# Kernel tuning notes

Hardware: AMD Instinct MI355X
Metric: run time of the kernel (lower is better)

Reference implementation:

```python
import jax, jax.numpy as jnp
import numpy as np


def setup_inputs() -> dict:
    key = jax.random.key(0)
    ks = jax.random.split(key, 8)
    B, C, H, W = 8, 256, 64, 64
    s = 1.0 / np.sqrt(C)
    return {
        "x": jax.random.normal(ks[0], (B, C, H, W), dtype=jnp.float32),
        "wq": jax.random.normal(ks[1], (C, C), dtype=jnp.float32) * s,
        "bq": jax.random.normal(ks[2], (C,), dtype=jnp.float32) * 0.01,
        "wk": jax.random.normal(ks[3], (C, C), dtype=jnp.float32) * s,
        "bk": jax.random.normal(ks[4], (C,), dtype=jnp.float32) * 0.01,
        "wv": jax.random.normal(ks[5], (C, C), dtype=jnp.float32) * s,
        "bv": jax.random.normal(ks[6], (C,), dtype=jnp.float32) * 0.01,
        "gamma": jax.random.normal(ks[7], (1,), dtype=jnp.float32) * 0.1,
    }


def reference(x, wq, bq, wk, bk, wv, bv, gamma):
    B, C, H, W = x.shape
    N = H * W
    xf = x.reshape(B, C, N)  # flatten spatial -> tokens
    # 1x1 convs == per-pixel linear maps over channels
    q = jnp.einsum('oc,bcn->bon', wq, xf) + bq[None, :, None]  # [B,C,N]
    k = jnp.einsum('oc,bcn->bon', wk, xf) + bk[None, :, None]  # [B,C,N]
    v = jnp.einsum('oc,bcn->bon', wv, xf) + bv[None, :, None]  # [B,C,N]
    # energy[b,n,m] = <q[:, n], k[:, m]>  (query tokens x key tokens)
    energy = jnp.einsum('bcn,bcm->bnm', q, k)  # [B,N,N]
    attention = jax.nn.softmax(energy, axis=-1)
    # out = V @ attention^T : out[b,c,n] = sum_m v[b,c,m] * attention[b,n,m]
    out = jnp.einsum('bcm,bnm->bcn', v, attention).reshape(B, C, H, W)
    return gamma[0] * out + x
```

## Files before the change

kernel.cpp:

```cpp
#include <hip/hip_runtime.h>
#include <hip/hip_bf16.h>
#include <cstdint>


typedef short short8 __attribute__((ext_vector_type(8)));
typedef short short4v __attribute__((ext_vector_type(4)));
typedef float f32x4 __attribute__((ext_vector_type(4)));

#define MFMA16(a, b, c) __builtin_amdgcn_mfma_f32_16x16x32_bf16((a), (b), (c), 0, 0, 0)
#define LOG2E 1.4426950408889634f

__device__ __forceinline__ unsigned short f2bf(float f) {
    union { float f; unsigned int u; } v;
    v.f = f;
    unsigned int u = v.u;
    return (unsigned short)((u + 0x7fffu + ((u >> 16) & 1u)) >> 16);
}

__device__ __forceinline__ void load_lds16(const unsigned short* g, unsigned short* l) {
    __builtin_amdgcn_global_load_lds(
        (const __attribute__((address_space(1))) unsigned int*)g,
        (__attribute__((address_space(3))) unsigned int*)l, 16, 0, 0);
}

__device__ __forceinline__ float rowmax16_dpp(float x) {
    int v;
    v = __builtin_amdgcn_update_dpp(0, __float_as_int(x), 0x121, 0xf, 0xf, false);
    x = fmaxf(x, __int_as_float(v));
    v = __builtin_amdgcn_update_dpp(0, __float_as_int(x), 0x122, 0xf, 0xf, false);
    x = fmaxf(x, __int_as_float(v));
    v = __builtin_amdgcn_update_dpp(0, __float_as_int(x), 0x124, 0xf, 0xf, false);
    x = fmaxf(x, __int_as_float(v));
    v = __builtin_amdgcn_update_dpp(0, __float_as_int(x), 0x128, 0xf, 0xf, false);
    x = fmaxf(x, __int_as_float(v));
    return x;
}

__global__ __launch_bounds__(256) void wcvt_kernel(
    const float* __restrict__ wq, const float* __restrict__ wk,
    const float* __restrict__ wv, unsigned short* __restrict__ Wb)
{
    int idx = (blockIdx.x * 256 + threadIdx.x) * 4;
    const float* src = (idx < 65536) ? wq : ((idx < 131072) ? wk : wv);
    float4 f = *(const float4*)(src + (idx & 65535));
    short4v s = { (short)f2bf(f.x), (short)f2bf(f.y), (short)f2bf(f.z), (short)f2bf(f.w) };
    *(short4v*)(Wb + idx) = s;
}

__global__ __launch_bounds__(256, 2) void qkv_kernel(
    const float* __restrict__ x, const unsigned short* __restrict__ Wb,
    const float* __restrict__ bq, const float* __restrict__ bk,
    const float* __restrict__ bv,
    unsigned short* __restrict__ Qc, unsigned short* __restrict__ Kr,
    unsigned short* __restrict__ Vc)
{
    const int C = 256, N = 4096;
    __shared__ __align__(16) unsigned short Xt[32][264];

    const int tid  = threadIdx.x;
    const int bid  = blockIdx.x;
    const int b    = bid >> 7;
    const int n0   = (bid & 127) * 32;
    const int wave = tid >> 6;
    const int lane = tid & 63;
    const int quad = lane >> 4;
    const int l16  = lane & 15;
    const int ch0  = wave * 64;

    {
        const int token = tid & 31;
        const int cg    = tid >> 5;
        const float* xb = x + ((size_t)b * C) * N + n0 + token;
#pragma unroll
        for (int p = 0; p < 8; p++) {
            int c0 = p * 32 + cg * 4;
            float f0 = xb[(size_t)(c0 + 0) * N];
            float f1 = xb[(size_t)(c0 + 1) * N];
            float f2 = xb[(size_t)(c0 + 2) * N];
            float f3 = xb[(size_t)(c0 + 3) * N];
            short4v s = { (short)f2bf(f0), (short)f2bf(f1), (short)f2bf(f2), (short)f2bf(f3) };
            *(short4v*)(&Xt[token][c0]) = s;
        }
    }
    __syncthreads();

    f32x4 acc[3][4][2];
#pragma unroll
    for (int m = 0; m < 3; m++)
#pragma unroll
        for (int ct = 0; ct < 4; ct++)
#pragma unroll
            for (int tt = 0; tt < 2; tt++) acc[m][ct][tt] = (f32x4){0.f, 0.f, 0.f, 0.f};

#pragma unroll
    for (int kc = 0; kc < 8; kc++) {
        const int ko = kc * 32 + quad * 8;
        short8 ax0 = *(const short8*)(&Xt[l16][ko]);
        short8 ax1 = *(const short8*)(&Xt[16 + l16][ko]);
#pragma unroll
        for (int m = 0; m < 3; m++) {
#pragma unroll
            for (int ct = 0; ct < 4; ct++) {
                short8 wf = *(const short8*)(Wb + ((size_t)m << 16) +
                                             (ch0 + ct * 16 + l16) * 256 + ko);
                acc[m][ct][0] = MFMA16(ax0, wf, acc[m][ct][0]);
                acc[m][ct][1] = MFMA16(ax1, wf, acc[m][ct][1]);
            }
        }
    }

#pragma unroll
    for (int ct = 0; ct < 4; ct++) {
        const int ch = ch0 + ct * 16 + l16;
        const float biq = bq[ch], biv = bv[ch];
#pragma unroll
        for (int tt = 0; tt < 2; tt++) {
            const int tok0 = n0 + tt * 16 + quad * 4;
            short4v qs = { (short)f2bf((acc[0][ct][tt][0] + biq) * LOG2E),
                           (short)f2bf((acc[0][ct][tt][1] + biq) * LOG2E),
                           (short)f2bf((acc[0][ct][tt][2] + biq) * LOG2E),
                           (short)f2bf((acc[0][ct][tt][3] + biq) * LOG2E) };
            *(short4v*)(Qc + ((size_t)b * C + ch) * N + tok0) = qs;
            short4v vs = { (short)f2bf(acc[2][ct][tt][0] + biv),
                           (short)f2bf(acc[2][ct][tt][1] + biv),
                           (short)f2bf(acc[2][ct][tt][2] + biv),
                           (short)f2bf(acc[2][ct][tt][3] + biv) };
            *(short4v*)(Vc + ((size_t)b * C + ch) * N + tok0) = vs;
        }
    }

    __syncthreads();
#pragma unroll
    for (int ct = 0; ct < 4; ct++) {
        const int ch = ch0 + ct * 16 + l16;
        const float bik = bk[ch];
#pragma unroll
        for (int tt = 0; tt < 2; tt++) {
#pragma unroll
            for (int r = 0; r < 4; r++)
                Xt[tt * 16 + quad * 4 + r][ch] = f2bf(acc[1][ct][tt][r] + bik);
        }
    }
    __syncthreads();
#pragma unroll
    for (int p = 0; p < 2; p++) {
        int chunk = p * 256 + tid;
        int tok = chunk >> 4;
        int cc  = (chunk & 15) * 16;
        *(short8*)(Kr + ((size_t)b * N + n0 + tok) * C + cc) = *(const short8*)(&Xt[tok][cc]);
    }
}

__global__ __launch_bounds__(512, 2) void attn_kernel(
    const unsigned short* __restrict__ Qc,
    const unsigned short* __restrict__ Kr,
    const unsigned short* __restrict__ Vc,
    const float* __restrict__ x,
    const float* __restrict__ gamma,
    float* __restrict__ out)
{
    const int C = 256, N = 4096;
    __shared__ __align__(16) unsigned short KV[2][32768];
    __shared__ __align__(16) unsigned short Pt[8][1280];
    __shared__ float MlL[4][32];
    __shared__ float MwL[4];

    const int tid  = threadIdx.x;
    const int wave = tid >> 6;
    const int ks   = wave >> 2;
    const int w4   = wave & 3;
    const int lane = tid & 63;
    const int quad = lane >> 4;
    const int l16  = lane & 15;
    const int bid  = blockIdx.x;
    const int b    = bid & 7;
    const int q0   = (bid >> 3) * 128 + w4 * 32;

    const unsigned short* kb  = Kr + (size_t)b * N * C;
    const unsigned short* vcb = Vc + (size_t)b * C * N;

    short8 aqL[8], aqH[8];
    {
        const unsigned short* qb = Qc + (size_t)b * C * N + q0 + l16;
#pragma unroll
        for (int f = 0; f < 8; f++) {
#pragma unroll
            for (int j = 0; j < 8; j++) {
                size_t co = (size_t)(f * 32 + quad * 8 + j) * N;
                aqL[f][j] = (short)qb[co];
                aqH[f][j] = (short)qb[co + 16];
            }
        }
    }

    f32x4 oL[16], oH[16];
#pragma unroll
    for (int t = 0; t < 16; t++) {
        oL[t] = (f32x4){0.f, 0.f, 0.f, 0.f};
        oH[t] = (f32x4){0.f, 0.f, 0.f, 0.f};
    }
    float m_w = -__builtin_inff();
    float l_p[2][4];
#pragma unroll
    for (int h = 0; h < 2; h++)
#pragma unroll
        for (int r = 0; r < 4; r++) l_p[h][r] = 0.f;

    auto stage = [&](int buf, int m0) {
        unsigned short* dst = &KV[buf][0];
#pragma unroll
        for (int p = 0; p < 4; p++) {
            int chunk = p * 512 + tid;
            int half = chunk >> 10;
            int idx  = chunk & 1023;
            int key = idx >> 5;
            int j = (idx & 31) ^ (key & 31);
            load_lds16(kb + (size_t)(half * 2048 + m0 + key) * C + j * 8,
                       dst + half * 16384 + idx * 8);
        }
#pragma unroll
        for (int p = 0; p < 4; p++) {
            int chunk = p * 512 + tid;
            int half = chunk >> 10;
            int idx  = chunk & 1023;
            int c = idx >> 2;
            int j = (idx & 3) ^ (c & 3);
            load_lds16(vcb + (size_t)c * N + half * 2048 + m0 + j * 8,
                       dst + half * 16384 + 8192 + idx * 8);
        }
    };

    stage(0, 0);
    __syncthreads();

    unsigned short* PtW = &Pt[wave][0];

    for (int it = 0; it < 64; ++it) {
        const int cur = it & 1;
        if (it < 63) stage(cur ^ 1, (it + 1) * 32);

        const unsigned short* Kb = &KV[cur][ks * 16384];
        const unsigned short* Vb = Kb + 8192;

        f32x4 sL0 = {0.f,0.f,0.f,0.f}, sL1 = {0.f,0.f,0.f,0.f};
        f32x4 sH0 = {0.f,0.f,0.f,0.f}, sH1 = {0.f,0.f,0.f,0.f};
#pragma unroll
        for (int f = 0; f < 8; f++) {
            const int j = f * 4 + quad;
            int k0 = l16, k1 = 16 + l16;
            short8 kf0 = *(const short8*)(Kb + (k0 * 32 + (j ^ (k0 & 31))) * 8);
            short8 kf1 = *(const short8*)(Kb + (k1 * 32 + (j ^ (k1 & 31))) * 8);
            sL0 = MFMA16(aqL[f], kf0, sL0);
            sL1 = MFMA16(aqL[f], kf1, sL1);
            sH0 = MFMA16(aqH[f], kf0, sH0);
            sH1 = MFMA16(aqH[f], kf1, sH1);
        }

        float mx = fmaxf(fmaxf(fmaxf(sL0[0], sL0[1]), fmaxf(sL0[2], sL0[3])),
                         fmaxf(fmaxf(sL1[0], sL1[1]), fmaxf(sL1[2], sL1[3])));
        mx = fmaxf(mx, fmaxf(fmaxf(fmaxf(sH0[0], sH0[1]), fmaxf(sH0[2], sH0[3])),
                             fmaxf(fmaxf(sH1[0], sH1[1]), fmaxf(sH1[2], sH1[3]))));
        mx = rowmax16_dpp(mx);
        mx = fmaxf(mx, __shfl_xor(mx, 16));
        mx = fmaxf(mx, __shfl_xor(mx, 32));
        const float mn = fmaxf(m_w, mx);
        const float al = exp2f(m_w - mn);
        const bool up = mn > m_w;
        m_w = mn;

#pragma unroll
        for (int r = 0; r < 4; r++) {
            {
                float e0 = exp2f(sL0[r] - mn);
                float e1 = exp2f(sL1[r] - mn);
                l_p[0][r] = l_p[0][r] * al + (e0 + e1);
                union { __hip_bfloat162 v; unsigned int u; } cv;
                cv.v = __float22bfloat162_rn(float2{e0, e1});
                unsigned short* pr = PtW + (quad * 4 + r) * 40 + l16;
                pr[0]  = (unsigned short)(cv.u & 0xffff);
                pr[16] = (unsigned short)(cv.u >> 16);
            }
            {
                float e0 = exp2f(sH0[r] - mn);
                float e1 = exp2f(sH1[r] - mn);
                l_p[1][r] = l_p[1][r] * al + (e0 + e1);
                union { __hip_bfloat162 v; unsigned int u; } cv;
                cv.v = __float22bfloat162_rn(float2{e0, e1});
                unsigned short* pr = PtW + (16 + quad * 4 + r) * 40 + l16;
                pr[0]  = (unsigned short)(cv.u & 0xffff);
                pr[16] = (unsigned short)(cv.u >> 16);
            }
        }
        if (up) {
#pragma unroll
            for (int t = 0; t < 16; t++) { oL[t] *= al; oH[t] *= al; }
        }

        short8 apL = *(const short8*)(PtW + l16 * 40 + quad * 8);
        short8 apH = *(const short8*)(PtW + (16 + l16) * 40 + quad * 8);

#pragma unroll
        for (int t = 0; t < 16; t++) {
            int c = t * 16 + l16;
            short8 vf = *(const short8*)(Vb + (c * 4 + (quad ^ (c & 3))) * 8);
            oL[t] = MFMA16(apL, vf, oL[t]);
            oH[t] = MFMA16(apH, vf, oH[t]);
        }
        __syncthreads();
    }

#pragma unroll
    for (int h = 0; h < 2; h++)
#pragma unroll
        for (int r = 0; r < 4; r++) {
            float rs = l_p[h][r];
            rs += __shfl_xor(rs, 1);
            rs += __shfl_xor(rs, 2);
            rs += __shfl_xor(rs, 4);
            rs += __shfl_xor(rs, 8);
            l_p[h][r] = rs;
        }

    float* CombF = (float*)(&KV[0][0]);
    __syncthreads();
    if (ks == 1) {
#pragma unroll
        for (int t = 0; t < 16; t++) {
#pragma unroll
            for (int r = 0; r < 4; r++) {
                CombF[(size_t)(w4 * 32 + quad * 4 + r) * 256 + t * 16 + l16] = oL[t][r];
                CombF[(size_t)(w4 * 32 + 16 + quad * 4 + r) * 256 + t * 16 + l16] = oH[t][r];
            }
        }
        if (l16 == 0) {
#pragma unroll
            for (int h = 0; h < 2; h++)
#pragma unroll
                for (int r = 0; r < 4; r++)
                    MlL[w4][h * 16 + quad * 4 + r] = l_p[h][r];
            if (lane == 0) MwL[w4] = m_w;
        }
    }
    __syncthreads();
    if (ks == 0) {
        const float g = gamma[0];
        const float m2w = MwL[w4];
        const float mt = fmaxf(m_w, m2w);
        const float f1 = exp2f(m_w - mt);
        const float f2 = exp2f(m2w - mt);
        float linv[2][4];
#pragma unroll
        for (int h = 0; h < 2; h++)
#pragma unroll
            for (int r = 0; r < 4; r++) {
                float l2 = MlL[w4][h * 16 + quad * 4 + r];
                linv[h][r] = g / (l_p[h][r] * f1 + l2 * f2);
            }
#pragma unroll
        for (int t = 0; t < 16; t++) {
            const int c = t * 16 + l16;
#pragma unroll
            for (int h = 0; h < 2; h++) {
                const int nb = q0 + h * 16 + quad * 4;
                f32x4 o1 = h ? oH[t] : oL[t];
                f32x4 ov;
#pragma unroll
                for (int r = 0; r < 4; r++) {
                    float o2 = CombF[(size_t)(w4 * 32 + h * 16 + quad * 4 + r) * 256 + c];
                    ov[r] = (o1[r] * f1 + o2 * f2) * linv[h][r];
                }
                size_t idx = ((size_t)(b * C + c)) * N + nb;
                f32x4 xv = *(const f32x4*)(x + idx);
                *(f32x4*)(out + idx) = ov + xv;
            }
        }
    }
}

extern "C" void kernel_launch(void* const* d_in, const int* in_sizes, int n_in,
                              void* d_out, int out_size, void* d_ws, size_t ws_size,
                              hipStream_t stream) {
    const int B = 8, C = 256, N = 4096;
    const float* x     = (const float*)d_in[0];
    const float* wq    = (const float*)d_in[1];
    const float* bq    = (const float*)d_in[2];
    const float* wk    = (const float*)d_in[3];
    const float* bk    = (const float*)d_in[4];
    const float* wv    = (const float*)d_in[5];
    const float* bv    = (const float*)d_in[6];
    const float* gamma = (const float*)d_in[7];
    float* out = (float*)d_out;

    unsigned short* Qc = (unsigned short*)d_ws;
    unsigned short* Kr = Qc + (size_t)B * C * N;
    unsigned short* Vc = Kr + (size_t)B * N * C;
    unsigned short* Wb = Vc + (size_t)B * C * N;

    wcvt_kernel<<<dim3(192), 256, 0, stream>>>(wq, wk, wv, Wb);
    qkv_kernel<<<dim3(1024), 256, 0, stream>>>(x, Wb, bq, bk, bv, Qc, Kr, Vc);
    attn_kernel<<<dim3(256), 512, 0, stream>>>(Qc, Kr, Vc, x, gamma, out);
}
```

Baseline: 393.6 us.

## Use per-row softmax max and pre-swizzle weights into MFMA fragment order

The attention kernel now keeps one running max per query row instead of one per wave. Each row's max is reduced with DPP only, which drops the cross-quad shuffles, and the output is rescaled with per-row factors only when some lane's max grows. The split-key combine now merges per-row maxes. Separately, the weight conversion kernel writes bf16 weights in MFMA fragment order, so the QKV kernel reads each fragment as one contiguous 512-element block with coalesced lane loads. Per-row maxes may trigger rescales more often, and the extra per-row exp2 work adds ALU cost.

```diff
diff --git a/kernel.cpp b/kernel.cpp
--- a/kernel.cpp
+++ b/kernel.cpp
@@ -38,17 +38,26 @@
 
 __global__ __launch_bounds__(256) void wcvt_kernel(
     const float* __restrict__ wq, const float* __restrict__ wk,
-    const float* __restrict__ wv, unsigned short* __restrict__ Wb)
+    const float* __restrict__ wv, unsigned short* __restrict__ W2)
 {
-    int idx = (blockIdx.x * 256 + threadIdx.x) * 4;
-    const float* src = (idx < 65536) ? wq : ((idx < 131072) ? wk : wv);
-    float4 f = *(const float4*)(src + (idx & 65535));
-    short4v s = { (short)f2bf(f.x), (short)f2bf(f.y), (short)f2bf(f.z), (short)f2bf(f.w) };
-    *(short4v*)(Wb + idx) = s;
+    int gid = blockIdx.x * 256 + threadIdx.x;
+    int lane = gid & 63;
+    int cht  = (gid >> 6) & 15;
+    int kc   = (gid >> 10) & 7;
+    int mat  = gid >> 13;
+    const float* src = (mat == 0) ? wq : ((mat == 1) ? wk : wv);
+    int ch = cht * 16 + (lane & 15);
+    int k  = kc * 32 + ((lane >> 4) & 3) * 8;
+    const float* s = src + ch * 256 + k;
+    float4 f0 = *(const float4*)(s);
+    float4 f1 = *(const float4*)(s + 4);
+    short8 o = { (short)f2bf(f0.x), (short)f2bf(f0.y), (short)f2bf(f0.z), (short)f2bf(f0.w),
+                 (short)f2bf(f1.x), (short)f2bf(f1.y), (short)f2bf(f1.z), (short)f2bf(f1.w) };
+    *(short8*)(W2 + (size_t)gid * 8) = o;
 }
 
 __global__ __launch_bounds__(256, 2) void qkv_kernel(
-    const float* __restrict__ x, const unsigned short* __restrict__ Wb,
+    const float* __restrict__ x, const unsigned short* __restrict__ W2,
     const float* __restrict__ bq, const float* __restrict__ bk,
     const float* __restrict__ bv,
     unsigned short* __restrict__ Qc, unsigned short* __restrict__ Kr,
@@ -101,8 +110,8 @@
         for (int m = 0; m < 3; m++) {
 #pragma unroll
             for (int ct = 0; ct < 4; ct++) {
-                short8 wf = *(const short8*)(Wb + ((size_t)m << 16) +
-                                             (ch0 + ct * 16 + l16) * 256 + ko);
+                int frag = ((m * 8 + kc) * 16 + wave * 4 + ct);
+                short8 wf = *(const short8*)(W2 + (size_t)frag * 512 + lane * 8);
                 acc[m][ct][0] = MFMA16(ax0, wf, acc[m][ct][0]);
                 acc[m][ct][1] = MFMA16(ax1, wf, acc[m][ct][1]);
             }
@@ -163,7 +172,7 @@
     __shared__ __align__(16) unsigned short KV[2][32768];
     __shared__ __align__(16) unsigned short Pt[8][1280];
     __shared__ float MlL[4][32];
-    __shared__ float MwL[4];
+    __shared__ float MmL[4][32];
 
     const int tid  = threadIdx.x;
     const int wave = tid >> 6;
@@ -199,12 +208,11 @@
         oL[t] = (f32x4){0.f, 0.f, 0.f, 0.f};
         oH[t] = (f32x4){0.f, 0.f, 0.f, 0.f};
     }
-    float m_w = -__builtin_inff();
-    float l_p[2][4];
+    float m_r[2][4], l_p[2][4];
 #pragma unroll
     for (int h = 0; h < 2; h++)
 #pragma unroll
-        for (int r = 0; r < 4; r++) l_p[h][r] = 0.f;
+        for (int r = 0; r < 4; r++) { m_r[h][r] = -__builtin_inff(); l_p[h][r] = 0.f; }
 
     auto stage = [&](int buf, int m0) {
         unsigned short* dst = &KV[buf][0];
@@ -256,21 +264,17 @@
             sH1 = MFMA16(aqH[f], kf1, sH1);
         }
 
-        float mx = fmaxf(fmaxf(fmaxf(sL0[0], sL0[1]), fmaxf(sL0[2], sL0[3])),
-                         fmaxf(fmaxf(sL1[0], sL1[1]), fmaxf(sL1[2], sL1[3])));
-        mx = fmaxf(mx, fmaxf(fmaxf(fmaxf(sH0[0], sH0[1]), fmaxf(sH0[2], sH0[3])),
-                             fmaxf(fmaxf(sH1[0], sH1[1]), fmaxf(sH1[2], sH1[3]))));
-        mx = rowmax16_dpp(mx);
-        mx = fmaxf(mx, __shfl_xor(mx, 16));
-        mx = fmaxf(mx, __shfl_xor(mx, 32));
-        const float mn = fmaxf(m_w, mx);
-        const float al = exp2f(m_w - mn);
-        const bool up = mn > m_w;
-        m_w = mn;
-
+        float aLr[4], aHr[4];
+        bool anyup = false;
 #pragma unroll
         for (int r = 0; r < 4; r++) {
             {
+                float mx = rowmax16_dpp(fmaxf(sL0[r], sL1[r]));
+                float mn = fmaxf(m_r[0][r], mx);
+                anyup |= (mn > m_r[0][r]);
+                float al = exp2f(m_r[0][r] - mn);
+                m_r[0][r] = mn;
+                aLr[r] = al;
                 float e0 = exp2f(sL0[r] - mn);
                 float e1 = exp2f(sL1[r] - mn);
                 l_p[0][r] = l_p[0][r] * al + (e0 + e1);
@@ -281,6 +285,12 @@
                 pr[16] = (unsigned short)(cv.u >> 16);
             }
             {
+                float mx = rowmax16_dpp(fmaxf(sH0[r], sH1[r]));
+                float mn = fmaxf(m_r[1][r], mx);
+                anyup |= (mn > m_r[1][r]);
+                float al = exp2f(m_r[1][r] - mn);
+                m_r[1][r] = mn;
+                aHr[r] = al;
                 float e0 = exp2f(sH0[r] - mn);
                 float e1 = exp2f(sH1[r] - mn);
                 l_p[1][r] = l_p[1][r] * al + (e0 + e1);
@@ -291,9 +301,11 @@
                 pr[16] = (unsigned short)(cv.u >> 16);
             }
         }
-        if (up) {
-#pragma unroll
-            for (int t = 0; t < 16; t++) { oL[t] *= al; oH[t] *= al; }
+        if (__any(anyup)) {
+            f32x4 aLv = (f32x4){aLr[0], aLr[1], aLr[2], aLr[3]};
+            f32x4 aHv = (f32x4){aHr[0], aHr[1], aHr[2], aHr[3]};
+#pragma unroll
+            for (int t = 0; t < 16; t++) { oL[t] *= aLv; oH[t] *= aHv; }
         }
 
         short8 apL = *(const short8*)(PtW + l16 * 40 + quad * 8);
@@ -336,24 +348,27 @@
 #pragma unroll
             for (int h = 0; h < 2; h++)
 #pragma unroll
-                for (int r = 0; r < 4; r++)
+                for (int r = 0; r < 4; r++) {
                     MlL[w4][h * 16 + quad * 4 + r] = l_p[h][r];
-            if (lane == 0) MwL[w4] = m_w;
+                    MmL[w4][h * 16 + quad * 4 + r] = m_r[h][r];
+                }
         }
     }
     __syncthreads();
     if (ks == 0) {
         const float g = gamma[0];
-        const float m2w = MwL[w4];
-        const float mt = fmaxf(m_w, m2w);
-        const float f1 = exp2f(m_w - mt);
-        const float f2 = exp2f(m2w - mt);
-        float linv[2][4];
+        float f1v[2][4], f2v[2][4], linv[2][4];
 #pragma unroll
         for (int h = 0; h < 2; h++)
 #pragma unroll
             for (int r = 0; r < 4; r++) {
+                float m2 = MmL[w4][h * 16 + quad * 4 + r];
                 float l2 = MlL[w4][h * 16 + quad * 4 + r];
+                float mt = fmaxf(m_r[h][r], m2);
+                float f1 = exp2f(m_r[h][r] - mt);
+                float f2 = exp2f(m2 - mt);
+                f1v[h][r] = f1;
+                f2v[h][r] = f2;
                 linv[h][r] = g / (l_p[h][r] * f1 + l2 * f2);
             }
 #pragma unroll
@@ -367,7 +382,7 @@
 #pragma unroll
                 for (int r = 0; r < 4; r++) {
                     float o2 = CombF[(size_t)(w4 * 32 + h * 16 + quad * 4 + r) * 256 + c];
-                    ov[r] = (o1[r] * f1 + o2 * f2) * linv[h][r];
+                    ov[r] = (o1[r] * f1v[h][r] + o2 * f2v[h][r]) * linv[h][r];
                 }
                 size_t idx = ((size_t)(b * C + c)) * N + nb;
                 f32x4 xv = *(const f32x4*)(x + idx);
@@ -394,9 +409,9 @@
     unsigned short* Qc = (unsigned short*)d_ws;
     unsigned short* Kr = Qc + (size_t)B * C * N;
     unsigned short* Vc = Kr + (size_t)B * N * C;
-    unsigned short* Wb = Vc + (size_t)B * C * N;
-
-    wcvt_kernel<<<dim3(192), 256, 0, stream>>>(wq, wk, wv, Wb);
-    qkv_kernel<<<dim3(1024), 256, 0, stream>>>(x, Wb, bq, bk, bv, Qc, Kr, Vc);
+    unsigned short* W2 = Vc + (size_t)B * C * N;
+
+    wcvt_kernel<<<dim3(96), 256, 0, stream>>>(wq, wk, wv, W2);
+    qkv_kernel<<<dim3(1024), 256, 0, stream>>>(x, W2, bq, bk, bv, Qc, Kr, Vc);
     attn_kernel<<<dim3(256), 512, 0, stream>>>(Qc, Kr, Vc, x, gamma, out);
 }
```

After: 510.4 us. 1.3x slower.
